# Performance work log

Measured on AMD Instinct MI355X. Metric: run time of the kernel, lower is better.

The kernel has to match this reference:

```python
import jax, jax.numpy as jnp
import numpy as np


def phi(x):
    return jax.nn.elu(x) + 1.0


def setup_inputs() -> dict:
    key = jax.random.key(0)
    ks = jax.random.split(key, 6)
    B, C, H, W = 16, 256, 64, 64
    scale = 1.0 / np.sqrt(C)
    x = jax.random.normal(ks[0], (B, C, H, W), dtype=jnp.float32)
    Wq = jax.random.normal(ks[1], (C, C), dtype=jnp.float32) * scale
    Wk = jax.random.normal(ks[2], (C, C), dtype=jnp.float32) * scale
    Wv = jax.random.normal(ks[3], (C, C), dtype=jnp.float32) * scale
    Wo = jax.random.normal(ks[4], (C, C), dtype=jnp.float32) * scale
    bo = jnp.zeros((C,), dtype=jnp.float32)
    return {"x": x, "Wq": Wq, "Wk": Wk, "Wv": Wv, "Wo": Wo, "bo": bo}


def reference(x, Wq, Wk, Wv, Wo, bo):
    # 1x1 convs == channel matmuls: out[b,o,h,w] = sum_c W[o,c] x[b,c,h,w]
    q = jnp.einsum('oc,bchw->bohw', Wq, x)
    k = jnp.einsum('oc,bchw->bohw', Wk, x)
    v = jnp.einsum('oc,bchw->bohw', Wv, x)
    phi_q, phi_k, phi_v = phi(q), phi(k), phi(v)
    # context matrix per batch: [B, C, C]
    qv = jnp.einsum('bchw,bdhw->bcd', phi_q, phi_v)
    # per-batch 1x1 conv with weight qv[b] applied to phi_k[b]
    attended = jnp.einsum('bcd,bdhw->bchw', qv, phi_k)
    # output projection with bias; dropout is identity at eval
    out = jnp.einsum('oc,bchw->bohw', Wo, attended) + bo[None, :, None, None]
    return out
```

## Files before the change

kernel.cpp:

```cpp
#include <hip/hip_runtime.h>
#include <hip/hip_bf16.h>


typedef short  bf16x8 __attribute__((ext_vector_type(8)));
typedef float  f32x4  __attribute__((ext_vector_type(4)));
typedef unsigned short u16x4 __attribute__((ext_vector_type(4)));

#define NB 16
#define NC 256
#define NN 4096

__device__ __forceinline__ unsigned short f2bf(float f) {
    union { float f; unsigned u; } v; v.f = f;
    unsigned r = v.u + 0x7FFFu + ((v.u >> 16) & 1u);
    return (unsigned short)(r >> 16);
}

__device__ __forceinline__ float phi_act(float v) {
    return v > 0.f ? v + 1.f : __expf(v);
}

__device__ __forceinline__ void gload_lds16(const void* g, void* l) {
    __builtin_amdgcn_global_load_lds(
        (const __attribute__((address_space(1))) void*)g,
        (__attribute__((address_space(3))) void*)l, 16, 0, 0);
}

__device__ __forceinline__ void stage_tile(
    const unsigned short* __restrict__ src, int ld, int kb, char* lds, int t)
{
    const int kslot  = t & 7;
    const int rbase  = t >> 3;
    const int srcOff = (kslot * 16) ^ ((rbase & 7) << 4);
    const int wbase  = (t >> 6) * 1024;
    #pragma unroll
    for (int i = 0; i < 4; ++i) {
        const int r = i * 32 + rbase;
        const char* g = (const char*)(src + (size_t)r * ld + kb) + srcOff;
        gload_lds16(g, lds + i * 4096 + wbase);
    }
}

__device__ __forceinline__ bf16x8 frag_ld(const char* lds, int row, int kbyte) {
    return *(const bf16x8*)(lds + row * 128 + (kbyte ^ ((row & 7) << 4)));
}

template<bool SWAP>
__device__ __forceinline__ void gemm128(
    const unsigned short* __restrict__ A, int lda,
    const unsigned short* __restrict__ BT, int ldb,
    int k0, int nk, char* lsA, char* lsB, f32x4 (&acc)[4][4])
{
    const int t = threadIdx.x;
    const int lane = t & 63;
    const int w  = t >> 6;
    const int wr = (w >> 1) * 64, wc = (w & 1) * 64;
    const int q  = lane >> 4, c15 = lane & 15;

    for (int kt = 0; kt < nk; ++kt) {
        const int kb = k0 + kt * 64;
        if (kt) __syncthreads();
        stage_tile(A,  lda, kb, lsA, t);
        stage_tile(BT, ldb, kb, lsB, t);
        __syncthreads();
        #pragma unroll
        for (int g = 0; g < 2; ++g) {
            const int kbyte = g * 64 + q * 16;
            bf16x8 af[4], bfr[4];
            #pragma unroll
            for (int m = 0; m < 4; ++m) af[m]  = frag_ld(lsA, wr + m * 16 + c15, kbyte);
            #pragma unroll
            for (int n = 0; n < 4; ++n) bfr[n] = frag_ld(lsB, wc + n * 16 + c15, kbyte);
            #pragma unroll
            for (int m = 0; m < 4; ++m)
                #pragma unroll
                for (int n = 0; n < 4; ++n)
                    acc[m][n] = SWAP
                        ? __builtin_amdgcn_mfma_f32_16x16x32_bf16(bfr[n], af[m], acc[m][n], 0, 0, 0)
                        : __builtin_amdgcn_mfma_f32_16x16x32_bf16(af[m], bfr[n], acc[m][n], 0, 0, 0);
        }
    }
}

__global__ __launch_bounds__(256) void k_pre(
    const float* __restrict__ x,
    const float* __restrict__ Wq, const float* __restrict__ Wk,
    const float* __restrict__ Wv, const float* __restrict__ Wo,
    unsigned short* __restrict__ xT,
    unsigned short* __restrict__ Wqkv, unsigned short* __restrict__ Wob)
{
    __shared__ float tile[64][68];
    const int id = blockIdx.x;
    if (id >= 4096) {
        int i = (id - 4096) * 256 + threadIdx.x;
        if      (i < 65536)  Wqkv[i] = f2bf(Wq[i]);
        else if (i < 131072) Wqkv[i] = f2bf(Wk[i - 65536]);
        else if (i < 196608) Wqkv[i] = f2bf(Wv[i - 131072]);
        else                 Wob[i - 196608] = f2bf(Wo[i - 196608]);
        return;
    }
    const int b  = id >> 8;
    const int n0 = (id & 63) * 64, c0 = ((id >> 6) & 3) * 64;
    const int t  = threadIdx.x;
    const float* xp = x + ((size_t)b * NC + c0) * NN + n0;
    const int cc = t >> 4, nq = t & 15;
    #pragma unroll
    for (int j = 0; j < 4; ++j) {
        const int c = j * 16 + cc;
        f32x4 v = *(const f32x4*)(xp + (size_t)c * NN + nq * 4);
        *(f32x4*)&tile[c][nq * 4] = v;
    }
    __syncthreads();
    unsigned short* op = xT + ((size_t)b * NN + n0) * NC + c0;
    const int nn0 = t >> 4, cq = t & 15;
    #pragma unroll
    for (int j = 0; j < 4; ++j) {
        const int nn = j * 16 + nn0;
        u16x4 o;
        #pragma unroll
        for (int ii = 0; ii < 4; ++ii) o[ii] = f2bf(tile[cq * 4 + ii][nn]);
        *(u16x4*)(op + (size_t)nn * NC + cq * 4) = o;
    }
}

__global__ __launch_bounds__(256) void k_proj(
    const unsigned short* __restrict__ Wqkv, const unsigned short* __restrict__ xT,
    unsigned short* __restrict__ phiQ, unsigned short* __restrict__ phiKT,
    unsigned short* __restrict__ phiV)
{
    __shared__ char lds[32768];
    const int bid = (blockIdx.x & 7) * 384 + (blockIdx.x >> 3);
    const int nt  = bid & 31;
    const int mt  = (bid >> 5) % 6;
    const int b   = bid / 192;
    const unsigned short* A  = Wqkv + mt * 128 * NC;
    const unsigned short* BT = xT + ((size_t)b * NN + nt * 128) * NC;

    const int lane = threadIdx.x & 63;
    const int w    = threadIdx.x >> 6;
    const int wr   = (w >> 1) * 64, wc = (w & 1) * 64;
    const int q4   = (lane >> 4) * 4, c15 = lane & 15;
    const int p    = mt >> 1;

    f32x4 acc[4][4] = {};
    if (p == 1) {
        gemm128<false>(A, NC, BT, NC, 0, 4, lds, lds + 16384, acc);
        unsigned short* dst = phiKT + (size_t)b * NN * NC;
        const int cb = (mt & 1) * 128 + wr + q4;
        const int nb = nt * 128 + wc + c15;
        #pragma unroll
        for (int m = 0; m < 4; ++m)
            #pragma unroll
            for (int n = 0; n < 4; ++n) {
                u16x4 pk;
                #pragma unroll
                for (int i = 0; i < 4; ++i) pk[i] = f2bf(phi_act(acc[m][n][i]));
                *(u16x4*)(dst + (size_t)(nb + n * 16) * NC + cb + m * 16) = pk;
            }
    } else {
        gemm128<true>(A, NC, BT, NC, 0, 4, lds, lds + 16384, acc);
        unsigned short* dst = (p == 0 ? phiQ : phiV) + (size_t)b * NC * NN;
        const int ob = (mt & 1) * 128 + wr + c15;
        const int nb = nt * 128 + wc + q4;
        #pragma unroll
        for (int m = 0; m < 4; ++m)
            #pragma unroll
            for (int n = 0; n < 4; ++n) {
                u16x4 pk;
                #pragma unroll
                for (int i = 0; i < 4; ++i) pk[i] = f2bf(phi_act(acc[m][n][i]));
                *(u16x4*)(dst + (size_t)(ob + m * 16) * NN + nb + n * 16) = pk;
            }
    }
}

__global__ __launch_bounds__(256) void k_qv(
    const unsigned short* __restrict__ phiQ, const unsigned short* __restrict__ phiV,
    float* __restrict__ qvTp)
{
    __shared__ char lds[32768];
    const int bid = (blockIdx.x & 7) * 64 + (blockIdx.x >> 3);
    const int s = bid & 7, nt = (bid >> 3) & 1, mt = (bid >> 4) & 1, b = bid >> 5;
    const unsigned short* A  = phiQ + ((size_t)b * NC + mt * 128) * NN;
    const unsigned short* BT = phiV + ((size_t)b * NC + nt * 128) * NN;
    f32x4 acc[4][4] = {};
    gemm128<false>(A, NN, BT, NN, s * 512, 8, lds, lds + 16384, acc);

    const int lane = threadIdx.x & 63, w = threadIdx.x >> 6;
    const int wr = (w >> 1) * 64, wc = (w & 1) * 64;
    const int q4 = (lane >> 4) * 4, c15 = lane & 15;
    float* dst = qvTp + (((size_t)s * NB + b) << 16);
    const int c0 = mt * 128 + wr + q4;
    const int d0 = nt * 128 + wc + c15;
    #pragma unroll
    for (int m = 0; m < 4; ++m)
        #pragma unroll
        for (int n = 0; n < 4; ++n)
            *(f32x4*)(dst + (size_t)(d0 + n * 16) * NC + c0 + m * 16) = acc[m][n];
}

__global__ __launch_bounds__(256) void k_qvred(
    const float* __restrict__ p, unsigned short* __restrict__ qvT)
{
    const size_t i = (size_t)blockIdx.x * 256 + threadIdx.x;
    const f32x4* pv = (const f32x4*)p;
    f32x4 v = pv[i];
    #pragma unroll
    for (int s = 1; s < 8; ++s) v = v + pv[i + (size_t)s * 262144];
    u16x4 o;
    #pragma unroll
    for (int j = 0; j < 4; ++j) o[j] = f2bf(v[j]);
    ((u16x4*)qvT)[i] = o;
}

__global__ __launch_bounds__(256) void k_mproj(
    const unsigned short* __restrict__ Wob, const unsigned short* __restrict__ qvT,
    unsigned short* __restrict__ Mb)
{
    __shared__ char lds[32768];
    const int bid = blockIdx.x;
    const int nt = bid & 1, mt = (bid >> 1) & 1, b = bid >> 2;
    const unsigned short* A  = Wob + mt * 128 * NC;
    const unsigned short* BT = qvT + ((size_t)b << 16) + nt * 128 * NC;
    f32x4 acc[4][4] = {};
    gemm128<true>(A, NC, BT, NC, 0, 4, lds, lds + 16384, acc);

    const int lane = threadIdx.x & 63, w = threadIdx.x >> 6;
    const int wr = (w >> 1) * 64, wc = (w & 1) * 64;
    const int q4 = (lane >> 4) * 4, c15 = lane & 15;
    unsigned short* dst = Mb + ((size_t)b << 16);
    const int ob = mt * 128 + wr + c15;
    const int db = nt * 128 + wc + q4;
    #pragma unroll
    for (int m = 0; m < 4; ++m)
        #pragma unroll
        for (int n = 0; n < 4; ++n) {
            u16x4 pk;
            #pragma unroll
            for (int i = 0; i < 4; ++i) pk[i] = f2bf(acc[m][n][i]);
            *(u16x4*)(dst + (size_t)(ob + m * 16) * NC + db + n * 16) = pk;
        }
}

__global__ __launch_bounds__(256) void k_out(
    const unsigned short* __restrict__ Mb, const unsigned short* __restrict__ phiKT,
    const float* __restrict__ bo, float* __restrict__ out)
{
    __shared__ char lds[32768];
    const int bid = blockIdx.x;
    const int nt = bid & 31, mt = (bid >> 5) & 1, b = bid >> 6;
    const unsigned short* A  = Mb + ((size_t)b << 16) + mt * 128 * NC;
    const unsigned short* BT = phiKT + (size_t)b * NN * NC + (size_t)nt * 128 * NC;
    f32x4 acc[4][4] = {};
    gemm128<true>(A, NC, BT, NC, 0, 4, lds, lds + 16384, acc);

    const int lane = threadIdx.x & 63, w = threadIdx.x >> 6;
    const int wr = (w >> 1) * 64, wc = (w & 1) * 64;
    const int q4 = (lane >> 4) * 4, c15 = lane & 15;
    float* dst = out + (size_t)b * NC * NN;
    #pragma unroll
    for (int m = 0; m < 4; ++m) {
        const int o  = mt * 128 + wr + m * 16 + c15;
        const float bb = bo[o];
        #pragma unroll
        for (int n = 0; n < 4; ++n) {
            f32x4 v = acc[m][n];
            #pragma unroll
            for (int i = 0; i < 4; ++i) v[i] += bb;
            *(f32x4*)(dst + (size_t)o * NN + nt * 128 + wc + n * 16 + q4) = v;
        }
    }
}

extern "C" void kernel_launch(void* const* d_in, const int* in_sizes, int n_in,
                              void* d_out, int out_size, void* d_ws, size_t ws_size,
                              hipStream_t stream)
{
    (void)in_sizes; (void)n_in; (void)out_size; (void)ws_size;
    const float* x  = (const float*)d_in[0];
    const float* Wq = (const float*)d_in[1];
    const float* Wk = (const float*)d_in[2];
    const float* Wv = (const float*)d_in[3];
    const float* Wo = (const float*)d_in[4];
    const float* bo = (const float*)d_in[5];
    float* out = (float*)d_out;

    char* ws = (char*)d_ws;
    size_t off = 0;
    auto alloc = [&](size_t bytes) {
        void* p = ws + off;
        off += (bytes + 255) & ~(size_t)255;
        return p;
    };
    unsigned short* xT    = (unsigned short*)alloc((size_t)NB * NN * NC * 2);
    unsigned short* phiQ  = (unsigned short*)alloc((size_t)NB * NC * NN * 2);
    unsigned short* phiV  = (unsigned short*)alloc((size_t)NB * NC * NN * 2);
    unsigned short* phiKT = (unsigned short*)alloc((size_t)NB * NN * NC * 2);
    unsigned short* qvT   = (unsigned short*)alloc((size_t)NB * NC * NC * 2);
    unsigned short* Mb    = (unsigned short*)alloc((size_t)NB * NC * NC * 2);
    unsigned short* Wqkv  = (unsigned short*)alloc((size_t)768 * NC * 2);
    unsigned short* Wob   = (unsigned short*)alloc((size_t)NC * NC * 2);
    float* qvTp = (float*)xT;

    k_pre<<<5120, 256, 0, stream>>>(x, Wq, Wk, Wv, Wo, xT, Wqkv, Wob);
    k_proj<<<3072, 256, 0, stream>>>(Wqkv, xT, phiQ, phiKT, phiV);
    k_qv<<<512, 256, 0, stream>>>(phiQ, phiV, qvTp);
    k_qvred<<<1024, 256, 0, stream>>>(qvTp, qvT);
    k_mproj<<<64, 256, 0, stream>>>(Wob, qvT, Mb);
    k_out<<<1024, 256, 0, stream>>>(Mb, phiKT, bo, out);
}
```

Measured before the change: 124.1 us.

## Keep weight fragments in registers and pipeline multiple N tiles per block

Adds a gemm routine that loads the full K=256 A (weight/Mb) fragments into registers once, then streams several 128-column B tiles through a double-buffered LDS pipeline with explicit vmcnt waits and barriers. The epilogue runs per N tile, so k_proj processes 4 tiles per block and k_out processes 2, cutting grid sizes and removing redundant A staging. Block-index swizzles in k_proj and k_qv are dropped. This raises register pressure (af holds 32 vectors), declared via launch_bounds occupancy 2, and gives fewer blocks for load balancing.

After: 130.1 us. +4.8%, slower.

```diff
diff --git a/kernel.cpp b/kernel.cpp
--- a/kernel.cpp
+++ b/kernel.cpp
@@ -9,6 +9,9 @@
 #define NB 16
 #define NC 256
 #define NN 4096
+
+#define WAITV(N) asm volatile("s_waitcnt vmcnt(" #N ")" ::: "memory")
+#define SCHED0() __builtin_amdgcn_sched_barrier(0)
 
 __device__ __forceinline__ unsigned short f2bf(float f) {
     union { float f; unsigned u; } v; v.f = f;
@@ -43,6 +46,79 @@
 
 __device__ __forceinline__ bf16x8 frag_ld(const char* lds, int row, int kbyte) {
     return *(const bf16x8*)(lds + row * 128 + (kbyte ^ ((row & 7) << 4)));
+}
+
+template<bool SWAP, int G, class Epi>
+__device__ __forceinline__ void gemm_k256_pipe(
+    const unsigned short* __restrict__ A,
+    const unsigned short* __restrict__ BT0, int ldb,
+    char* lds, Epi epi)
+{
+    const int t = threadIdx.x, lane = t & 63, w = t >> 6;
+    const int wr = (w >> 1) * 64, wc = (w & 1) * 64;
+    const int q = lane >> 4, c15 = lane & 15;
+
+    bf16x8 af[8][4];
+    {
+        const unsigned short* ab = A + (size_t)(wr + c15) * NC + q * 8;
+        #pragma unroll
+        for (int kg = 0; kg < 8; ++kg)
+            #pragma unroll
+            for (int m = 0; m < 4; ++m)
+                af[kg][m] = *(const bf16x8*)(ab + m * 16 * NC + kg * 32);
+    }
+
+    auto stage_s = [&](int s) {
+        stage_tile(BT0 + (size_t)(s >> 2) * 128 * ldb, ldb, (s & 3) * 64,
+                   lds + (s & 1) * 16384, t);
+    };
+    stage_s(0);
+    stage_s(1);
+
+    f32x4 acc[4][4] = {};
+    for (int nti = 0; nti < G; ++nti) {
+        #pragma unroll
+        for (int kt = 0; kt < 4; ++kt) {
+            const int s = nti * 4 + kt;
+            if (kt == 0) {
+                if (nti > 0) { WAITV(0); } else { WAITV(4); }
+            } else if (kt == 3) {
+                if (nti == G - 1) { WAITV(0); } else { WAITV(4); }
+            } else {
+                WAITV(4);
+            }
+            SCHED0();
+            __builtin_amdgcn_s_barrier();
+            SCHED0();
+            const char* cur = lds + (s & 1) * 16384;
+            #pragma unroll
+            for (int g = 0; g < 2; ++g) {
+                bf16x8 bfr[4];
+                #pragma unroll
+                for (int n = 0; n < 4; ++n)
+                    bfr[n] = frag_ld(cur, wc + n * 16 + c15, g * 64 + q * 16);
+                #pragma unroll
+                for (int m = 0; m < 4; ++m)
+                    #pragma unroll
+                    for (int n = 0; n < 4; ++n)
+                        acc[m][n] = SWAP
+                            ? __builtin_amdgcn_mfma_f32_16x16x32_bf16(bfr[n], af[kt * 2 + g][m], acc[m][n], 0, 0, 0)
+                            : __builtin_amdgcn_mfma_f32_16x16x32_bf16(af[kt * 2 + g][m], bfr[n], acc[m][n], 0, 0, 0);
+            }
+            SCHED0();
+            __builtin_amdgcn_s_barrier();
+            SCHED0();
+            if (s + 2 < 4 * G) stage_s(s + 2);
+            if (kt == 3) {
+                epi(nti, acc);
+                #pragma unroll
+                for (int m = 0; m < 4; ++m)
+                    #pragma unroll
+                    for (int n = 0; n < 4; ++n)
+                        acc[m][n] = f32x4{0.f, 0.f, 0.f, 0.f};
+            }
+        }
+    }
 }
 
 template<bool SWAP>
@@ -123,18 +199,16 @@
     }
 }
 
-__global__ __launch_bounds__(256) void k_proj(
+__global__ __launch_bounds__(256, 2) void k_proj(
     const unsigned short* __restrict__ Wqkv, const unsigned short* __restrict__ xT,
     unsigned short* __restrict__ phiQ, unsigned short* __restrict__ phiKT,
     unsigned short* __restrict__ phiV)
 {
-    __shared__ char lds[32768];
-    const int bid = (blockIdx.x & 7) * 384 + (blockIdx.x >> 3);
-    const int nt  = bid & 31;
-    const int mt  = (bid >> 5) % 6;
-    const int b   = bid / 192;
-    const unsigned short* A  = Wqkv + mt * 128 * NC;
-    const unsigned short* BT = xT + ((size_t)b * NN + nt * 128) * NC;
+    __shared__ __align__(16) char lds[32768];
+    const int bid = blockIdx.x;
+    const int ng = bid & 7, mt = (bid >> 3) % 6, b = bid / 48;
+    const unsigned short* A   = Wqkv + (size_t)mt * 128 * NC;
+    const unsigned short* BT0 = xT + ((size_t)b * NN + ng * 512) * NC;
 
     const int lane = threadIdx.x & 63;
     const int w    = threadIdx.x >> 6;
@@ -142,35 +216,38 @@
     const int q4   = (lane >> 4) * 4, c15 = lane & 15;
     const int p    = mt >> 1;
 
-    f32x4 acc[4][4] = {};
     if (p == 1) {
-        gemm128<false>(A, NC, BT, NC, 0, 4, lds, lds + 16384, acc);
         unsigned short* dst = phiKT + (size_t)b * NN * NC;
         const int cb = (mt & 1) * 128 + wr + q4;
-        const int nb = nt * 128 + wc + c15;
-        #pragma unroll
-        for (int m = 0; m < 4; ++m)
-            #pragma unroll
-            for (int n = 0; n < 4; ++n) {
-                u16x4 pk;
-                #pragma unroll
-                for (int i = 0; i < 4; ++i) pk[i] = f2bf(phi_act(acc[m][n][i]));
-                *(u16x4*)(dst + (size_t)(nb + n * 16) * NC + cb + m * 16) = pk;
-            }
+        gemm_k256_pipe<false, 4>(A, BT0, NC, lds,
+            [&](int nti, f32x4 (&acc)[4][4]) {
+                const int nb = ng * 512 + nti * 128 + wc + c15;
+                #pragma unroll
+                for (int m = 0; m < 4; ++m)
+                    #pragma unroll
+                    for (int n = 0; n < 4; ++n) {
+                        u16x4 pk;
+                        #pragma unroll
+                        for (int i = 0; i < 4; ++i) pk[i] = f2bf(phi_act(acc[m][n][i]));
+                        *(u16x4*)(dst + (size_t)(nb + n * 16) * NC + cb + m * 16) = pk;
+                    }
+            });
     } else {
-        gemm128<true>(A, NC, BT, NC, 0, 4, lds, lds + 16384, acc);
         unsigned short* dst = (p == 0 ? phiQ : phiV) + (size_t)b * NC * NN;
         const int ob = (mt & 1) * 128 + wr + c15;
-        const int nb = nt * 128 + wc + q4;
-        #pragma unroll
-        for (int m = 0; m < 4; ++m)
-            #pragma unroll
-            for (int n = 0; n < 4; ++n) {
-                u16x4 pk;
-                #pragma unroll
-                for (int i = 0; i < 4; ++i) pk[i] = f2bf(phi_act(acc[m][n][i]));
-                *(u16x4*)(dst + (size_t)(ob + m * 16) * NN + nb + n * 16) = pk;
-            }
+        gemm_k256_pipe<true, 4>(A, BT0, NC, lds,
+            [&](int nti, f32x4 (&acc)[4][4]) {
+                const int nb = ng * 512 + nti * 128 + wc + q4;
+                #pragma unroll
+                for (int m = 0; m < 4; ++m)
+                    #pragma unroll
+                    for (int n = 0; n < 4; ++n) {
+                        u16x4 pk;
+                        #pragma unroll
+                        for (int i = 0; i < 4; ++i) pk[i] = f2bf(phi_act(acc[m][n][i]));
+                        *(u16x4*)(dst + (size_t)(ob + m * 16) * NN + nb + n * 16) = pk;
+                    }
+            });
     }
 }
 
@@ -179,7 +256,7 @@
     float* __restrict__ qvTp)
 {
     __shared__ char lds[32768];
-    const int bid = (blockIdx.x & 7) * 64 + (blockIdx.x >> 3);
+    const int bid = blockIdx.x;
     const int s = bid & 7, nt = (bid >> 3) & 1, mt = (bid >> 4) & 1, b = bid >> 5;
     const unsigned short* A  = phiQ + ((size_t)b * NC + mt * 128) * NN;
     const unsigned short* BT = phiV + ((size_t)b * NC + nt * 128) * NN;
@@ -242,34 +319,36 @@
         }
 }
 
-__global__ __launch_bounds__(256) void k_out(
+__global__ __launch_bounds__(256, 2) void k_out(
     const unsigned short* __restrict__ Mb, const unsigned short* __restrict__ phiKT,
     const float* __restrict__ bo, float* __restrict__ out)
 {
-    __shared__ char lds[32768];
+    __shared__ __align__(16) char lds[32768];
     const int bid = blockIdx.x;
-    const int nt = bid & 31, mt = (bid >> 5) & 1, b = bid >> 6;
-    const unsigned short* A  = Mb + ((size_t)b << 16) + mt * 128 * NC;
-    const unsigned short* BT = phiKT + (size_t)b * NN * NC + (size_t)nt * 128 * NC;
-    f32x4 acc[4][4] = {};
-    gemm128<true>(A, NC, BT, NC, 0, 4, lds, lds + 16384, acc);
+    const int ng = bid & 15, mt = (bid >> 4) & 1, b = bid >> 5;
+    const unsigned short* A   = Mb + ((size_t)b << 16) + (size_t)mt * 128 * NC;
+    const unsigned short* BT0 = phiKT + (size_t)b * NN * NC + (size_t)ng * 256 * NC;
+    float* dst = out + (size_t)b * NC * NN;
 
     const int lane = threadIdx.x & 63, w = threadIdx.x >> 6;
     const int wr = (w >> 1) * 64, wc = (w & 1) * 64;
     const int q4 = (lane >> 4) * 4, c15 = lane & 15;
-    float* dst = out + (size_t)b * NC * NN;
-    #pragma unroll
-    for (int m = 0; m < 4; ++m) {
-        const int o  = mt * 128 + wr + m * 16 + c15;
-        const float bb = bo[o];
-        #pragma unroll
-        for (int n = 0; n < 4; ++n) {
-            f32x4 v = acc[m][n];
-            #pragma unroll
-            for (int i = 0; i < 4; ++i) v[i] += bb;
-            *(f32x4*)(dst + (size_t)o * NN + nt * 128 + wc + n * 16 + q4) = v;
-        }
-    }
+
+    gemm_k256_pipe<true, 2>(A, BT0, NC, lds,
+        [&](int nti, f32x4 (&acc)[4][4]) {
+            #pragma unroll
+            for (int m = 0; m < 4; ++m) {
+                const int o = mt * 128 + wr + m * 16 + c15;
+                const float bb = bo[o];
+                #pragma unroll
+                for (int n = 0; n < 4; ++n) {
+                    f32x4 v = acc[m][n];
+                    #pragma unroll
+                    for (int i = 0; i < 4; ++i) v[i] += bb;
+                    *(f32x4*)(dst + (size_t)o * NN + ng * 256 + nti * 128 + wc + n * 16 + q4) = v;
+                }
+            }
+        });
 }
 
 extern "C" void kernel_launch(void* const* d_in, const int* in_sizes, int n_in,
@@ -303,9 +382,9 @@
     float* qvTp = (float*)xT;
 
     k_pre<<<5120, 256, 0, stream>>>(x, Wq, Wk, Wv, Wo, xT, Wqkv, Wob);
-    k_proj<<<3072, 256, 0, stream>>>(Wqkv, xT, phiQ, phiKT, phiV);
+    k_proj<<<768, 256, 0, stream>>>(Wqkv, xT, phiQ, phiKT, phiV);
     k_qv<<<512, 256, 0, stream>>>(phiQ, phiV, qvTp);
     k_qvred<<<1024, 256, 0, stream>>>(qvTp, qvT);
     k_mproj<<<64, 256, 0, stream>>>(Wob, qvT, Mb);
-    k_out<<<1024, 256, 0, stream>>>(Mb, phiKT, bo, out);
-}
+    k_out<<<512, 256, 0, stream>>>(Mb, phiKT, bo, out);
+}
```

## Widen proj and out GEMM tiles to 128x256 and drop block swizzle

Applied to the files above, without the earlier changes.

Adds a GEMM helper that computes 128x256 output tiles with K fixed at 256. Each wave now holds a 64x128 accumulator (4x8 MFMA fragments), and the B operand is staged with 256 rows in 32 KB of LDS. k_proj and k_out use it, which halves their grid sizes and raises reuse of the A tile per block, at the cost of more registers and LDS (48 KB, launch bounds of 2 blocks per CU). The XCD-aware blockIdx remapping is removed from k_proj and k_qv, which may change L2 locality.

New measurement: 126.8 us. +2.1%, slower.

```diff
diff --git a/kernel.cpp b/kernel.cpp
--- a/kernel.cpp
+++ b/kernel.cpp
@@ -26,6 +26,7 @@
         (__attribute__((address_space(3))) void*)l, 16, 0, 0);
 }
 
+template<int NR>
 __device__ __forceinline__ void stage_tile(
     const unsigned short* __restrict__ src, int ld, int kb, char* lds, int t)
 {
@@ -34,7 +35,7 @@
     const int srcOff = (kslot * 16) ^ ((rbase & 7) << 4);
     const int wbase  = (t >> 6) * 1024;
     #pragma unroll
-    for (int i = 0; i < 4; ++i) {
+    for (int i = 0; i < NR / 32; ++i) {
         const int r = i * 32 + rbase;
         const char* g = (const char*)(src + (size_t)r * ld + kb) + srcOff;
         gload_lds16(g, lds + i * 4096 + wbase);
@@ -43,6 +44,42 @@
 
 __device__ __forceinline__ bf16x8 frag_ld(const char* lds, int row, int kbyte) {
     return *(const bf16x8*)(lds + row * 128 + (kbyte ^ ((row & 7) << 4)));
+}
+
+template<bool SWAP, class Epi>
+__device__ __forceinline__ void gemm_k256_w256(
+    const unsigned short* __restrict__ A,
+    const unsigned short* __restrict__ BT,
+    char* lsA, char* lsB, Epi epi)
+{
+    const int t = threadIdx.x, lane = t & 63, w = t >> 6;
+    const int wr = (w >> 1) * 64, wc = (w & 1) * 128;
+    const int q = lane >> 4, c15 = lane & 15;
+
+    f32x4 acc[4][8] = {};
+    for (int kt = 0; kt < 4; ++kt) {
+        if (kt) __syncthreads();
+        stage_tile<128>(A,  NC, kt * 64, lsA, t);
+        stage_tile<256>(BT, NC, kt * 64, lsB, t);
+        __syncthreads();
+        #pragma unroll
+        for (int g = 0; g < 2; ++g) {
+            const int kbyte = g * 64 + q * 16;
+            bf16x8 afr[4], bfr[8];
+            #pragma unroll
+            for (int m = 0; m < 4; ++m) afr[m] = frag_ld(lsA, wr + m * 16 + c15, kbyte);
+            #pragma unroll
+            for (int n = 0; n < 8; ++n) bfr[n] = frag_ld(lsB, wc + n * 16 + c15, kbyte);
+            #pragma unroll
+            for (int m = 0; m < 4; ++m)
+                #pragma unroll
+                for (int n = 0; n < 8; ++n)
+                    acc[m][n] = SWAP
+                        ? __builtin_amdgcn_mfma_f32_16x16x32_bf16(bfr[n], afr[m], acc[m][n], 0, 0, 0)
+                        : __builtin_amdgcn_mfma_f32_16x16x32_bf16(afr[m], bfr[n], acc[m][n], 0, 0, 0);
+        }
+    }
+    epi(acc);
 }
 
 template<bool SWAP>
@@ -60,8 +97,8 @@
     for (int kt = 0; kt < nk; ++kt) {
         const int kb = k0 + kt * 64;
         if (kt) __syncthreads();
-        stage_tile(A,  lda, kb, lsA, t);
-        stage_tile(BT, ldb, kb, lsB, t);
+        stage_tile<128>(A,  lda, kb, lsA, t);
+        stage_tile<128>(BT, ldb, kb, lsB, t);
         __syncthreads();
         #pragma unroll
         for (int g = 0; g < 2; ++g) {
@@ -123,54 +160,55 @@
     }
 }
 
-__global__ __launch_bounds__(256) void k_proj(
+__global__ __launch_bounds__(256, 2) void k_proj(
     const unsigned short* __restrict__ Wqkv, const unsigned short* __restrict__ xT,
     unsigned short* __restrict__ phiQ, unsigned short* __restrict__ phiKT,
     unsigned short* __restrict__ phiV)
 {
-    __shared__ char lds[32768];
-    const int bid = (blockIdx.x & 7) * 384 + (blockIdx.x >> 3);
-    const int nt  = bid & 31;
-    const int mt  = (bid >> 5) % 6;
-    const int b   = bid / 192;
-    const unsigned short* A  = Wqkv + mt * 128 * NC;
-    const unsigned short* BT = xT + ((size_t)b * NN + nt * 128) * NC;
+    __shared__ __align__(16) char lds[49152];
+    const int bid = blockIdx.x;
+    const int ng = bid & 15, mt = (bid >> 4) % 6, b = bid / 96;
+    const unsigned short* A  = Wqkv + (size_t)mt * 128 * NC;
+    const unsigned short* BT = xT + ((size_t)b * NN + ng * 256) * NC;
 
     const int lane = threadIdx.x & 63;
     const int w    = threadIdx.x >> 6;
-    const int wr   = (w >> 1) * 64, wc = (w & 1) * 64;
+    const int wr   = (w >> 1) * 64, wc = (w & 1) * 128;
     const int q4   = (lane >> 4) * 4, c15 = lane & 15;
     const int p    = mt >> 1;
 
-    f32x4 acc[4][4] = {};
     if (p == 1) {
-        gemm128<false>(A, NC, BT, NC, 0, 4, lds, lds + 16384, acc);
         unsigned short* dst = phiKT + (size_t)b * NN * NC;
         const int cb = (mt & 1) * 128 + wr + q4;
-        const int nb = nt * 128 + wc + c15;
-        #pragma unroll
-        for (int m = 0; m < 4; ++m)
-            #pragma unroll
-            for (int n = 0; n < 4; ++n) {
-                u16x4 pk;
-                #pragma unroll
-                for (int i = 0; i < 4; ++i) pk[i] = f2bf(phi_act(acc[m][n][i]));
-                *(u16x4*)(dst + (size_t)(nb + n * 16) * NC + cb + m * 16) = pk;
-            }
+        const int nb = ng * 256 + wc + c15;
+        gemm_k256_w256<false>(A, BT, lds, lds + 16384,
+            [&](f32x4 (&acc)[4][8]) {
+                #pragma unroll
+                for (int m = 0; m < 4; ++m)
+                    #pragma unroll
+                    for (int n = 0; n < 8; ++n) {
+                        u16x4 pk;
+                        #pragma unroll
+                        for (int i = 0; i < 4; ++i) pk[i] = f2bf(phi_act(acc[m][n][i]));
+                        *(u16x4*)(dst + (size_t)(nb + n * 16) * NC + cb + m * 16) = pk;
+                    }
+            });
     } else {
-        gemm128<true>(A, NC, BT, NC, 0, 4, lds, lds + 16384, acc);
         unsigned short* dst = (p == 0 ? phiQ : phiV) + (size_t)b * NC * NN;
         const int ob = (mt & 1) * 128 + wr + c15;
-        const int nb = nt * 128 + wc + q4;
-        #pragma unroll
-        for (int m = 0; m < 4; ++m)
-            #pragma unroll
-            for (int n = 0; n < 4; ++n) {
-                u16x4 pk;
-                #pragma unroll
-                for (int i = 0; i < 4; ++i) pk[i] = f2bf(phi_act(acc[m][n][i]));
-                *(u16x4*)(dst + (size_t)(ob + m * 16) * NN + nb + n * 16) = pk;
-            }
+        const int nb = ng * 256 + wc + q4;
+        gemm_k256_w256<true>(A, BT, lds, lds + 16384,
+            [&](f32x4 (&acc)[4][8]) {
+                #pragma unroll
+                for (int m = 0; m < 4; ++m)
+                    #pragma unroll
+                    for (int n = 0; n < 8; ++n) {
+                        u16x4 pk;
+                        #pragma unroll
+                        for (int i = 0; i < 4; ++i) pk[i] = f2bf(phi_act(acc[m][n][i]));
+                        *(u16x4*)(dst + (size_t)(ob + m * 16) * NN + nb + n * 16) = pk;
+                    }
+            });
     }
 }
 
@@ -179,7 +217,7 @@
     float* __restrict__ qvTp)
 {
     __shared__ char lds[32768];
-    const int bid = (blockIdx.x & 7) * 64 + (blockIdx.x >> 3);
+    const int bid = blockIdx.x;
     const int s = bid & 7, nt = (bid >> 3) & 1, mt = (bid >> 4) & 1, b = bid >> 5;
     const unsigned short* A  = phiQ + ((size_t)b * NC + mt * 128) * NN;
     const unsigned short* BT = phiV + ((size_t)b * NC + nt * 128) * NN;
@@ -242,34 +280,36 @@
         }
 }
 
-__global__ __launch_bounds__(256) void k_out(
+__global__ __launch_bounds__(256, 2) void k_out(
     const unsigned short* __restrict__ Mb, const unsigned short* __restrict__ phiKT,
     const float* __restrict__ bo, float* __restrict__ out)
 {
-    __shared__ char lds[32768];
+    __shared__ __align__(16) char lds[49152];
     const int bid = blockIdx.x;
-    const int nt = bid & 31, mt = (bid >> 5) & 1, b = bid >> 6;
-    const unsigned short* A  = Mb + ((size_t)b << 16) + mt * 128 * NC;
-    const unsigned short* BT = phiKT + (size_t)b * NN * NC + (size_t)nt * 128 * NC;
-    f32x4 acc[4][4] = {};
-    gemm128<true>(A, NC, BT, NC, 0, 4, lds, lds + 16384, acc);
+    const int ng = bid & 15, mt = (bid >> 4) & 1, b = bid >> 5;
+    const unsigned short* A  = Mb + ((size_t)b << 16) + (size_t)mt * 128 * NC;
+    const unsigned short* BT = phiKT + (size_t)b * NN * NC + (size_t)ng * 256 * NC;
+    float* dst = out + (size_t)b * NC * NN;
 
     const int lane = threadIdx.x & 63, w = threadIdx.x >> 6;
-    const int wr = (w >> 1) * 64, wc = (w & 1) * 64;
+    const int wr = (w >> 1) * 64, wc = (w & 1) * 128;
     const int q4 = (lane >> 4) * 4, c15 = lane & 15;
-    float* dst = out + (size_t)b * NC * NN;
-    #pragma unroll
-    for (int m = 0; m < 4; ++m) {
-        const int o  = mt * 128 + wr + m * 16 + c15;
-        const float bb = bo[o];
-        #pragma unroll
-        for (int n = 0; n < 4; ++n) {
-            f32x4 v = acc[m][n];
-            #pragma unroll
-            for (int i = 0; i < 4; ++i) v[i] += bb;
-            *(f32x4*)(dst + (size_t)o * NN + nt * 128 + wc + n * 16 + q4) = v;
-        }
-    }
+
+    gemm_k256_w256<true>(A, BT, lds, lds + 16384,
+        [&](f32x4 (&acc)[4][8]) {
+            #pragma unroll
+            for (int m = 0; m < 4; ++m) {
+                const int o = mt * 128 + wr + m * 16 + c15;
+                const float bb = bo[o];
+                #pragma unroll
+                for (int n = 0; n < 8; ++n) {
+                    f32x4 v = acc[m][n];
+                    #pragma unroll
+                    for (int i = 0; i < 4; ++i) v[i] += bb;
+                    *(f32x4*)(dst + (size_t)o * NN + ng * 256 + wc + n * 16 + q4) = v;
+                }
+            }
+        });
 }
 
 extern "C" void kernel_launch(void* const* d_in, const int* in_sizes, int n_in,
@@ -303,9 +343,9 @@
     float* qvTp = (float*)xT;
 
     k_pre<<<5120, 256, 0, stream>>>(x, Wq, Wk, Wv, Wo, xT, Wqkv, Wob);
-    k_proj<<<3072, 256, 0, stream>>>(Wqkv, xT, phiQ, phiKT, phiV);
+    k_proj<<<1536, 256, 0, stream>>>(Wqkv, xT, phiQ, phiKT, phiV);
     k_qv<<<512, 256, 0, stream>>>(phiQ, phiV, qvTp);
     k_qvred<<<1024, 256, 0, stream>>>(qvTp, qvT);
     k_mproj<<<64, 256, 0, stream>>>(Wob, qvT, Mb);
-    k_out<<<1024, 256, 0, stream>>>(Mb, phiKT, bo, out);
-}
+    k_out<<<512, 256, 0, stream>>>(Mb, phiKT, bo, out);
+}
```

## Widen k_out tile to all 256 output channels and drop block swizzles

Applied to the files above, without the earlier changes.

k_out now computes a full 256x128 output tile per block, so each phiKT tile is loaded once instead of twice. The grid halves to 512 blocks, LDS grows to 48KB, and each wave holds 32 accumulators. Separately, the XCD-aware block index remapping in k_proj and k_qv is removed in favour of plain blockIdx ordering. Both changes shift register pressure, occupancy and L2 locality.

Result: no change. 125.6 us (+1.2%).

```diff
diff --git a/kernel.cpp b/kernel.cpp
--- a/kernel.cpp
+++ b/kernel.cpp
@@ -26,6 +26,7 @@
         (__attribute__((address_space(3))) void*)l, 16, 0, 0);
 }
 
+template<int NR>
 __device__ __forceinline__ void stage_tile(
     const unsigned short* __restrict__ src, int ld, int kb, char* lds, int t)
 {
@@ -34,7 +35,7 @@
     const int srcOff = (kslot * 16) ^ ((rbase & 7) << 4);
     const int wbase  = (t >> 6) * 1024;
     #pragma unroll
-    for (int i = 0; i < 4; ++i) {
+    for (int i = 0; i < NR / 32; ++i) {
         const int r = i * 32 + rbase;
         const char* g = (const char*)(src + (size_t)r * ld + kb) + srcOff;
         gload_lds16(g, lds + i * 4096 + wbase);
@@ -60,8 +61,8 @@
     for (int kt = 0; kt < nk; ++kt) {
         const int kb = k0 + kt * 64;
         if (kt) __syncthreads();
-        stage_tile(A,  lda, kb, lsA, t);
-        stage_tile(BT, ldb, kb, lsB, t);
+        stage_tile<128>(A,  lda, kb, lsA, t);
+        stage_tile<128>(BT, ldb, kb, lsB, t);
         __syncthreads();
         #pragma unroll
         for (int g = 0; g < 2; ++g) {
@@ -129,11 +130,11 @@
     unsigned short* __restrict__ phiV)
 {
     __shared__ char lds[32768];
-    const int bid = (blockIdx.x & 7) * 384 + (blockIdx.x >> 3);
+    const int bid = blockIdx.x;
     const int nt  = bid & 31;
     const int mt  = (bid >> 5) % 6;
     const int b   = bid / 192;
-    const unsigned short* A  = Wqkv + mt * 128 * NC;
+    const unsigned short* A  = Wqkv + (size_t)mt * 128 * NC;
     const unsigned short* BT = xT + ((size_t)b * NN + nt * 128) * NC;
 
     const int lane = threadIdx.x & 63;
@@ -179,7 +180,7 @@
     float* __restrict__ qvTp)
 {
     __shared__ char lds[32768];
-    const int bid = (blockIdx.x & 7) * 64 + (blockIdx.x >> 3);
+    const int bid = blockIdx.x;
     const int s = bid & 7, nt = (bid >> 3) & 1, mt = (bid >> 4) & 1, b = bid >> 5;
     const unsigned short* A  = phiQ + ((size_t)b * NC + mt * 128) * NN;
     const unsigned short* BT = phiV + ((size_t)b * NC + nt * 128) * NN;
@@ -246,28 +247,52 @@
     const unsigned short* __restrict__ Mb, const unsigned short* __restrict__ phiKT,
     const float* __restrict__ bo, float* __restrict__ out)
 {
-    __shared__ char lds[32768];
+    __shared__ __align__(16) char lds[49152];
+    char* lsA = lds;
+    char* lsB = lds + 32768;
     const int bid = blockIdx.x;
-    const int nt = bid & 31, mt = (bid >> 5) & 1, b = bid >> 6;
-    const unsigned short* A  = Mb + ((size_t)b << 16) + mt * 128 * NC;
-    const unsigned short* BT = phiKT + (size_t)b * NN * NC + (size_t)nt * 128 * NC;
-    f32x4 acc[4][4] = {};
-    gemm128<true>(A, NC, BT, NC, 0, 4, lds, lds + 16384, acc);
-
-    const int lane = threadIdx.x & 63, w = threadIdx.x >> 6;
-    const int wr = (w >> 1) * 64, wc = (w & 1) * 64;
-    const int q4 = (lane >> 4) * 4, c15 = lane & 15;
+    const int ng = bid & 31, b = bid >> 5;
+    const unsigned short* A  = Mb + ((size_t)b << 16);
+    const unsigned short* BT = phiKT + ((size_t)b * NN + ng * 128) * NC;
     float* dst = out + (size_t)b * NC * NN;
+
+    const int t = threadIdx.x, lane = t & 63, w = t >> 6;
+    const int wr = w * 64;
+    const int q = lane >> 4, c15 = lane & 15;
+
+    f32x4 acc[4][8] = {};
+    for (int kt = 0; kt < 4; ++kt) {
+        if (kt) __syncthreads();
+        stage_tile<256>(A,  NC, kt * 64, lsA, t);
+        stage_tile<128>(BT, NC, kt * 64, lsB, t);
+        __syncthreads();
+        #pragma unroll
+        for (int g = 0; g < 2; ++g) {
+            const int kbyte = g * 64 + q * 16;
+            bf16x8 afr[4], bfr[8];
+            #pragma unroll
+            for (int m = 0; m < 4; ++m) afr[m] = frag_ld(lsA, wr + m * 16 + c15, kbyte);
+            #pragma unroll
+            for (int n = 0; n < 8; ++n) bfr[n] = frag_ld(lsB, n * 16 + c15, kbyte);
+            #pragma unroll
+            for (int m = 0; m < 4; ++m)
+                #pragma unroll
+                for (int n = 0; n < 8; ++n)
+                    acc[m][n] = __builtin_amdgcn_mfma_f32_16x16x32_bf16(
+                        bfr[n], afr[m], acc[m][n], 0, 0, 0);
+        }
+    }
+    const int q4 = q * 4;
     #pragma unroll
     for (int m = 0; m < 4; ++m) {
-        const int o  = mt * 128 + wr + m * 16 + c15;
+        const int o = wr + m * 16 + c15;
         const float bb = bo[o];
         #pragma unroll
-        for (int n = 0; n < 4; ++n) {
+        for (int n = 0; n < 8; ++n) {
             f32x4 v = acc[m][n];
             #pragma unroll
             for (int i = 0; i < 4; ++i) v[i] += bb;
-            *(f32x4*)(dst + (size_t)o * NN + nt * 128 + wc + n * 16 + q4) = v;
+            *(f32x4*)(dst + (size_t)o * NN + ng * 128 + n * 16 + q4) = v;
         }
     }
 }
@@ -307,5 +332,5 @@
     k_qv<<<512, 256, 0, stream>>>(phiQ, phiV, qvTp);
     k_qvred<<<1024, 256, 0, stream>>>(qvTp, qvT);
     k_mproj<<<64, 256, 0, stream>>>(Wob, qvT, Mb);
-    k_out<<<1024, 256, 0, stream>>>(Mb, phiKT, bo, out);
-}
+    k_out<<<512, 256, 0, stream>>>(Mb, phiKT, bo, out);
+}
```
